# Kernel tuning notes

Hardware: AMD Instinct MI355X
Metric: run time of the kernel (lower is better)

## Reference

```python
import jax, jax.numpy as jnp
import numpy as np

DIM = 1024
HEADS = 16

def setup_inputs() -> dict:
    key = jax.random.key(0)
    ks = jax.random.split(key, 5)
    x = jax.random.normal(ks[0], (4, 2048, DIM), dtype=jnp.float32)
    s = 1.0 / np.sqrt(DIM)
    Wqkv = jax.random.normal(ks[1], (DIM, 3 * DIM), dtype=jnp.float32) * s
    bqkv = jnp.zeros((3 * DIM,), dtype=jnp.float32)
    Wproj = jax.random.normal(ks[2], (DIM, DIM), dtype=jnp.float32) * s
    bproj = jnp.zeros((DIM,), dtype=jnp.float32)
    return {"x": x, "Wqkv": Wqkv, "bqkv": bqkv, "Wproj": Wproj, "bproj": bproj}

def reference(x, Wqkv, bqkv, Wproj, bproj):
    B, N, D = x.shape
    H = HEADS
    hd = D // H
    scale = hd ** (-0.5)
    qkv = x @ Wqkv + bqkv                      # [B, N, 3D]
    q, k, v = jnp.split(qkv, 3, axis=-1)
    # [B, N, H, hd] -> [B, H, N, hd]
    q = q.reshape(B, N, H, hd).transpose(0, 2, 1, 3)
    k = k.reshape(B, N, H, hd).transpose(0, 2, 1, 3)
    v = v.reshape(B, N, H, hd).transpose(0, 2, 1, 3)
    attn = jnp.einsum('bhqd,bhkd->bhqk', q, k) * scale
    attn = jax.nn.softmax(attn, axis=-1)
    out = jnp.einsum('bhqk,bhkd->bhqd', attn, v)
    out = out.transpose(0, 2, 1, 3).reshape(B, N, D)
    return out @ Wproj + bproj
```

## Files before the change

kernel.cpp:

```cpp
#include <hip/hip_runtime.h>
#include <hip/hip_bf16.h>
#include <math.h>


typedef __bf16 bf16;
typedef __bf16 bf16x4 __attribute__((ext_vector_type(4)));
typedef __bf16 bf16x8 __attribute__((ext_vector_type(8)));
typedef float f32x4 __attribute__((ext_vector_type(4)));

#define AS1(p) ((const __attribute__((address_space(1))) void*)(p))
#define AS3(p) ((__attribute__((address_space(3))) void*)(p))

__device__ __forceinline__ void async16(const void* g, void* l) {
    __builtin_amdgcn_global_load_lds(AS1(g), AS3(l), 16, 0, 0);
}

#if __has_builtin(__builtin_amdgcn_exp2f)
#define EXP2(x) __builtin_amdgcn_exp2f(x)
#else
#define EXP2(x) exp2f(x)
#endif

#define QSCALE 0.18033688011112042f


__global__ void cvt_f32_bf16(const float* __restrict__ in, bf16* __restrict__ out, int n4) {
    int i = blockIdx.x * blockDim.x + threadIdx.x;
    if (i < n4) {
        float4 v = ((const float4*)in)[i];
        bf16x4 o;
        o.x = (bf16)v.x; o.y = (bf16)v.y; o.z = (bf16)v.z; o.w = (bf16)v.w;
        ((bf16x4*)out)[i] = o;
    }
}

__global__ void transpose_cvt(const float* __restrict__ in, bf16* __restrict__ out, int K, int N) {
    __shared__ float t[32][33];
    const int n0 = blockIdx.x * 32, k0 = blockIdx.y * 32;
    const int tx = threadIdx.x, ty = threadIdx.y;
    #pragma unroll
    for (int j = 0; j < 32; j += 8)
        t[ty + j][tx] = in[(size_t)(k0 + ty + j) * N + n0 + tx];
    __syncthreads();
    #pragma unroll
    for (int j = 0; j < 32; j += 8)
        out[(size_t)(n0 + ty + j) * K + k0 + tx] = (bf16)t[tx][ty + j];
}


__device__ __forceinline__ void gemm_mainloop(const bf16* __restrict__ A,
                                              const bf16* __restrict__ Bt,
                                              int K, int m0, int n0,
                                              bf16* As, bf16* Bs, f32x4 acc[4][4]) {
    const int tid = threadIdx.x;
    const int wave = tid >> 6, lane = tid & 63;
    const int c = lane & 15, quad = lane >> 4;
    const int wm = (wave & 1) * 64, wn = (wave >> 1) * 64;

    const int ci0 = (wave * 2 + 0) * 64 + lane;
    const int ci1 = (wave * 2 + 1) * 64 + lane;
    const bf16* ga0 = A  + (size_t)(m0 + (ci0 >> 2)) * K + (ci0 & 3) * 8;
    const bf16* ga1 = A  + (size_t)(m0 + (ci1 >> 2)) * K + (ci1 & 3) * 8;
    const bf16* gb0 = Bt + (size_t)(n0 + (ci0 >> 2)) * K + (ci0 & 3) * 8;
    const bf16* gb1 = Bt + (size_t)(n0 + (ci1 >> 2)) * K + (ci1 & 3) * 8;
    bf16* la0 = As + (wave * 2 + 0) * 512;
    bf16* la1 = As + (wave * 2 + 1) * 512;
    bf16* lb0 = Bs + (wave * 2 + 0) * 512;
    bf16* lb1 = Bs + (wave * 2 + 1) * 512;

    for (int kt = 0; kt < K; kt += 32) {
        async16(ga0 + kt, la0);
        async16(ga1 + kt, la1);
        async16(gb0 + kt, lb0);
        async16(gb1 + kt, lb1);
        __syncthreads();
        bf16x8 af[4], bfr[4];
        #pragma unroll
        for (int i = 0; i < 4; i++)
            af[i] = *(const bf16x8*)(As + (wm + i * 16 + c) * 32 + quad * 8);
        #pragma unroll
        for (int j = 0; j < 4; j++)
            bfr[j] = *(const bf16x8*)(Bs + (wn + j * 16 + c) * 32 + quad * 8);
        #pragma unroll
        for (int i = 0; i < 4; i++)
            #pragma unroll
            for (int j = 0; j < 4; j++)
                acc[i][j] = __builtin_amdgcn_mfma_f32_16x16x32_bf16(af[i], bfr[j], acc[i][j], 0, 0, 0);
        __syncthreads();
    }
}


__global__ __launch_bounds__(256) void gemm_qkv(const bf16* __restrict__ A,
                                                const bf16* __restrict__ Bt,
                                                const float* __restrict__ bias,
                                                bf16* __restrict__ Qb,
                                                bf16* __restrict__ Kb,
                                                bf16* __restrict__ Vtb) {
    __shared__ __align__(16) bf16 As[128 * 32];
    __shared__ __align__(16) bf16 Bs[128 * 32];
    f32x4 acc[4][4] = {};
    const int m0 = blockIdx.x * 128, n0 = blockIdx.y * 128;
    gemm_mainloop(A, Bt, 1024, m0, n0, As, Bs, acc);

    const int tid = threadIdx.x;
    const int wave = tid >> 6, lane = tid & 63;
    const int c = lane & 15, quad = lane >> 4;
    const int wm = (wave & 1) * 64, wn = (wave >> 1) * 64;
    const int sel = n0 >> 10;
    bf16* QK = (sel == 0) ? Qb : Kb;
    const float qs = (sel == 0) ? QSCALE : 1.0f;

    #pragma unroll
    for (int j = 0; j < 4; j++) {
        const int nfull = n0 + wn + j * 16 + c;
        const int nmod = nfull & 1023;
        const int h = nmod >> 6, e = nmod & 63;
        const float bv = bias[nfull];
        #pragma unroll
        for (int i = 0; i < 4; i++) {
            const int mbase = m0 + wm + i * 16 + quad * 4;
            const int b = mbase >> 11, t = mbase & 2047;
            if (sel < 2) {
                bf16* dst = QK + (((size_t)(b * 16 + h) * 2048 + t) * 64 + e);
                #pragma unroll
                for (int r = 0; r < 4; r++)
                    dst[(size_t)r * 64] = (bf16)((acc[i][j][r] + bv) * qs);
            } else {
                bf16* dst = Vtb + ((size_t)(b * 16 + h) * 64 + e) * 2048 + t;
                bf16x4 v;
                v.x = (bf16)(acc[i][j][0] + bv);
                v.y = (bf16)(acc[i][j][1] + bv);
                v.z = (bf16)(acc[i][j][2] + bv);
                v.w = (bf16)(acc[i][j][3] + bv);
                *(bf16x4*)dst = v;
            }
        }
    }
}


#define ATTN_STAGE(B) do { \
    async16(kS0, kD0_##B); async16(kS1, kD1_##B); \
    async16(vS0, vD0_##B); async16(vS1, vD1_##B); \
    kS0 += 4096; kS1 += 4096; vS0 += 64; vS1 += 64; \
} while (0)

#define ATTN_COMPUTE(B) do { \
    _Pragma("unroll") \
    for (int j = 0; j < 4; j++) { \
        bf16x8 kf0 = *(const bf16x8*)(kb0_##B + j * 1024); \
        bf16x8 kf1 = *(const bf16x8*)(kb1_##B + j * 1024); \
        f32x4 s0 = {}, s1 = {}; \
        __builtin_amdgcn_s_setprio(1); \
        s0 = __builtin_amdgcn_mfma_f32_16x16x32_bf16(kf0, qf[0][0], s0, 0, 0, 0); \
        s0 = __builtin_amdgcn_mfma_f32_16x16x32_bf16(kf1, qf[0][1], s0, 0, 0, 0); \
        s1 = __builtin_amdgcn_mfma_f32_16x16x32_bf16(kf0, qf[1][0], s1, 0, 0, 0); \
        s1 = __builtin_amdgcn_mfma_f32_16x16x32_bf16(kf1, qf[1][1], s1, 0, 0, 0); \
        __builtin_amdgcn_s_setprio(0); \
        _Pragma("unroll") \
        for (int r = 0; r < 4; r++) { s0[r] = EXP2(s0[r]); s1[r] = EXP2(s1[r]); } \
        lsum[0] += s0; \
        lsum[1] += s1; \
        bf16x4 p0, p1; \
        p0.x = (bf16)s0[0]; p0.y = (bf16)s0[1]; p0.z = (bf16)s0[2]; p0.w = (bf16)s0[3]; \
        p1.x = (bf16)s1[0]; p1.y = (bf16)s1[1]; p1.z = (bf16)s1[2]; p1.w = (bf16)s1[3]; \
        *(bf16x4*)(pwa + j * 16) = p0; \
        *(bf16x4*)(pwb + j * 16) = p1; \
    } \
    _Pragma("unroll") \
    for (int gks = 0; gks < 2; gks++) { \
        const bf16* vbg = gks ? vb1_##B : vb0_##B; \
        bf16x8 vf[4]; \
        _Pragma("unroll") \
        for (int n2 = 0; n2 < 4; n2++) \
            vf[n2] = *(const bf16x8*)(vbg + n2 * 1024); \
        bf16x8 pf0 = *(const bf16x8*)(pra + gks * 32); \
        bf16x8 pf1 = *(const bf16x8*)(prb + gks * 32); \
        __builtin_amdgcn_s_setprio(1); \
        _Pragma("unroll") \
        for (int n2 = 0; n2 < 4; n2++) { \
            o[0][n2] = __builtin_amdgcn_mfma_f32_16x16x32_bf16(pf0, vf[n2], o[0][n2], 0, 0, 0); \
            o[1][n2] = __builtin_amdgcn_mfma_f32_16x16x32_bf16(pf1, vf[n2], o[1][n2], 0, 0, 0); \
        } \
        __builtin_amdgcn_s_setprio(0); \
    } \
} while (0)

__global__ __launch_bounds__(256, 3) void attn_kernel(const bf16* __restrict__ Q,
                                                      const bf16* __restrict__ Kg,
                                                      const bf16* __restrict__ Vt,
                                                      bf16* __restrict__ Out) {
    __shared__ __align__(16) bf16 Ks0[64 * 64];
    __shared__ __align__(16) bf16 Ks1[64 * 64];
    __shared__ __align__(16) bf16 Vs0[64 * 64];
    __shared__ __align__(16) bf16 Vs1[64 * 64];
    __shared__ __align__(16) bf16 Pl[4 * 2 * 16 * 72];

    const int bh = blockIdx.x, qt = blockIdx.y;
    const int tid = threadIdx.x;
    const int wave = tid >> 6, lane = tid & 63;
    const int c = lane & 15, quad = lane >> 4;

    const bf16* Qb = Q + (size_t)bh * 2048 * 64;
    bf16* pw = Pl + wave * 2304;

    const int qbase = qt * 128 + wave * 32;

    bf16x8 qf[2][2];
    #pragma unroll
    for (int i = 0; i < 2; i++)
        #pragma unroll
        for (int ks = 0; ks < 2; ks++)
            qf[i][ks] = *(const bf16x8*)(Qb + (size_t)(qbase + i * 16 + c) * 64 + ks * 32 + quad * 8);

    const int s0i = tid, s1i = 256 + tid;
    const int rk0 = s0i >> 3, cg0 = (s0i & 7) ^ (rk0 & 7);
    const int rk1 = s1i >> 3, cg1 = (s1i & 7) ^ (rk1 & 7);
    const bf16* kS0 = Kg + (size_t)bh * 2048 * 64 + rk0 * 64 + cg0 * 8;
    const bf16* kS1 = Kg + (size_t)bh * 2048 * 64 + rk1 * 64 + cg1 * 8;
    const bf16* vS0 = Vt + (size_t)bh * 64 * 2048 + (size_t)rk0 * 2048 + cg0 * 8;
    const bf16* vS1 = Vt + (size_t)bh * 64 * 2048 + (size_t)rk1 * 2048 + cg1 * 8;
    bf16* kD0_0 = Ks0 + (size_t)(wave * 64) * 8;
    bf16* kD1_0 = Ks0 + (size_t)(256 + wave * 64) * 8;
    bf16* kD0_1 = Ks1 + (size_t)(wave * 64) * 8;
    bf16* kD1_1 = Ks1 + (size_t)(256 + wave * 64) * 8;
    bf16* vD0_0 = Vs0 + (size_t)(wave * 64) * 8;
    bf16* vD1_0 = Vs0 + (size_t)(256 + wave * 64) * 8;
    bf16* vD0_1 = Vs1 + (size_t)(wave * 64) * 8;
    bf16* vD1_1 = Vs1 + (size_t)(256 + wave * 64) * 8;

    const int sw = c & 7;
    const int ch0 = (quad ^ sw) * 8, ch1 = ((quad ^ sw) ^ 4) * 8;
    const bf16* kb0_0 = Ks0 + c * 64 + ch0;
    const bf16* kb1_0 = Ks0 + c * 64 + ch1;
    const bf16* kb0_1 = Ks1 + c * 64 + ch0;
    const bf16* kb1_1 = Ks1 + c * 64 + ch1;
    const bf16* vb0_0 = Vs0 + c * 64 + ch0;
    const bf16* vb1_0 = Vs0 + c * 64 + ch1;
    const bf16* vb0_1 = Vs1 + c * 64 + ch0;
    const bf16* vb1_1 = Vs1 + c * 64 + ch1;
    bf16* pwa = pw + c * 72 + quad * 4;
    bf16* pwb = pwa + 16 * 72;
    const bf16* pra = pw + c * 72 + quad * 8;
    const bf16* prb = pra + 16 * 72;

    f32x4 lsum[2] = {};
    f32x4 o[2][4] = {};

    ATTN_STAGE(0);
    __syncthreads();
    for (int kv2 = 0; kv2 < 16; kv2++) {
        ATTN_STAGE(1);
        ATTN_COMPUTE(0);
        __syncthreads();
        if (kv2 < 15) ATTN_STAGE(0);
        ATTN_COMPUTE(1);
        __syncthreads();
    }

    const int b = bh >> 4, hh = bh & 15;
    #pragma unroll
    for (int i = 0; i < 2; i++) {
        float lh = (lsum[i][0] + lsum[i][1]) + (lsum[i][2] + lsum[i][3]);
        lh += __shfl_xor(lh, 16);
        lh += __shfl_xor(lh, 32);
        const float li0 = __shfl(lh, quad * 4 + 0);
        const float li1 = __shfl(lh, quad * 4 + 1);
        const float li2 = __shfl(lh, quad * 4 + 2);
        const float li3 = __shfl(lh, quad * 4 + 3);
        const float inv[4] = {1.f / li0, 1.f / li1, 1.f / li2, 1.f / li3};
        #pragma unroll
        for (int r = 0; r < 4; r++) {
            const int token = b * 2048 + qbase + i * 16 + quad * 4 + r;
            #pragma unroll
            for (int n2 = 0; n2 < 4; n2++) {
                const int feat = hh * 64 + n2 * 16 + c;
                Out[(size_t)token * 1024 + feat] = (bf16)(o[i][n2][r] * inv[r]);
            }
        }
    }
}


__global__ __launch_bounds__(256) void gemm_proj(const bf16* __restrict__ A,
                                                 const bf16* __restrict__ Bt,
                                                 const float* __restrict__ bias,
                                                 float* __restrict__ Out) {
    __shared__ __align__(16) bf16 As[128 * 32];
    __shared__ __align__(16) bf16 Bs[128 * 32];
    f32x4 acc[4][4] = {};
    const int m0 = blockIdx.x * 128, n0 = blockIdx.y * 128;
    gemm_mainloop(A, Bt, 1024, m0, n0, As, Bs, acc);

    const int tid = threadIdx.x;
    const int wave = tid >> 6, lane = tid & 63;
    const int c = lane & 15, quad = lane >> 4;
    const int wm = (wave & 1) * 64, wn = (wave >> 1) * 64;

    #pragma unroll
    for (int j = 0; j < 4; j++) {
        const int nn = n0 + wn + j * 16 + c;
        const float bv = bias[nn];
        #pragma unroll
        for (int i = 0; i < 4; i++) {
            const int m = m0 + wm + i * 16 + quad * 4;
            #pragma unroll
            for (int r = 0; r < 4; r++)
                Out[(size_t)(m + r) * 1024 + nn] = acc[i][j][r] + bv;
        }
    }
}


extern "C" void kernel_launch(void* const* d_in, const int* in_sizes, int n_in,
                              void* d_out, int out_size, void* d_ws, size_t ws_size,
                              hipStream_t stream) {
    const float* x     = (const float*)d_in[0];
    const float* Wqkv  = (const float*)d_in[1];
    const float* bqkv  = (const float*)d_in[2];
    const float* Wproj = (const float*)d_in[3];
    const float* bproj = (const float*)d_in[4];
    float* out = (float*)d_out;

    char* ws = (char*)d_ws;
    bf16* xb     = (bf16*)(ws);
    bf16* wqkvt  = (bf16*)(ws + 16777216);
    bf16* wprojt = (bf16*)(ws + 23068672);
    bf16* Qb     = (bf16*)(ws + 25165824);
    bf16* Kb     = (bf16*)(ws + 41943040);
    bf16* Vtb    = (bf16*)(ws + 58720256);
    bf16* attno  = xb;

    cvt_f32_bf16<<<8192, 256, 0, stream>>>(x, xb, 2097152);
    transpose_cvt<<<dim3(96, 32), dim3(32, 8), 0, stream>>>(Wqkv, wqkvt, 1024, 3072);
    transpose_cvt<<<dim3(32, 32), dim3(32, 8), 0, stream>>>(Wproj, wprojt, 1024, 1024);
    gemm_qkv<<<dim3(64, 24), 256, 0, stream>>>(xb, wqkvt, bqkv, Qb, Kb, Vtb);
    attn_kernel<<<dim3(64, 16), 256, 0, stream>>>(Qb, Kb, Vtb, attno);
    gemm_proj<<<dim3(64, 8), 256, 0, stream>>>(attno, wprojt, bproj, out);
}
```

Baseline: 272.2 us.

## Double-buffer LDS tiles in GEMM mainloop to overlap loads with MFMA

The shared GEMM mainloop used by the QKV and projection kernels now keeps two LDS buffers for each of A and B. It issues the async global-to-LDS loads for the next K-slab before running the MFMAs on the current one, with the loop unrolled by two. This is meant to hide global load latency behind compute, where before each iteration waited on its own loads. In exchange, each block uses twice as much LDS, which may lower occupancy, and the overlap depends on the compiler placing the vmcnt wait at the barrier.

After: 272.6 us. About the same (+0.1%).

```diff
diff --git a/kernel.cpp b/kernel.cpp
--- a/kernel.cpp
+++ b/kernel.cpp
@@ -48,10 +48,32 @@
 }
 
 
+#define GEMM_STAGE(B) do { \
+    async16(ga0, la0_##B); async16(ga1, la1_##B); \
+    async16(gb0, lb0_##B); async16(gb1, lb1_##B); \
+    ga0 += 32; ga1 += 32; gb0 += 32; gb1 += 32; \
+} while (0)
+
+#define GEMM_COMPUTE(B) do { \
+    bf16x8 af[4], bfr[4]; \
+    _Pragma("unroll") \
+    for (int i = 0; i < 4; i++) \
+        af[i] = *(const bf16x8*)(As##B + (wm + i * 16 + c) * 32 + quad * 8); \
+    _Pragma("unroll") \
+    for (int j = 0; j < 4; j++) \
+        bfr[j] = *(const bf16x8*)(Bs##B + (wn + j * 16 + c) * 32 + quad * 8); \
+    _Pragma("unroll") \
+    for (int i = 0; i < 4; i++) \
+        _Pragma("unroll") \
+        for (int j = 0; j < 4; j++) \
+            acc[i][j] = __builtin_amdgcn_mfma_f32_16x16x32_bf16(af[i], bfr[j], acc[i][j], 0, 0, 0); \
+} while (0)
+
 __device__ __forceinline__ void gemm_mainloop(const bf16* __restrict__ A,
                                               const bf16* __restrict__ Bt,
                                               int K, int m0, int n0,
-                                              bf16* As, bf16* Bs, f32x4 acc[4][4]) {
+                                              bf16* As0, bf16* As1,
+                                              bf16* Bs0, bf16* Bs1, f32x4 acc[4][4]) {
     const int tid = threadIdx.x;
     const int wave = tid >> 6, lane = tid & 63;
     const int c = lane & 15, quad = lane >> 4;
@@ -63,29 +85,24 @@
     const bf16* ga1 = A  + (size_t)(m0 + (ci1 >> 2)) * K + (ci1 & 3) * 8;
     const bf16* gb0 = Bt + (size_t)(n0 + (ci0 >> 2)) * K + (ci0 & 3) * 8;
     const bf16* gb1 = Bt + (size_t)(n0 + (ci1 >> 2)) * K + (ci1 & 3) * 8;
-    bf16* la0 = As + (wave * 2 + 0) * 512;
-    bf16* la1 = As + (wave * 2 + 1) * 512;
-    bf16* lb0 = Bs + (wave * 2 + 0) * 512;
-    bf16* lb1 = Bs + (wave * 2 + 1) * 512;
-
-    for (int kt = 0; kt < K; kt += 32) {
-        async16(ga0 + kt, la0);
-        async16(ga1 + kt, la1);
-        async16(gb0 + kt, lb0);
-        async16(gb1 + kt, lb1);
+    bf16* la0_0 = As0 + (wave * 2 + 0) * 512;
+    bf16* la1_0 = As0 + (wave * 2 + 1) * 512;
+    bf16* la0_1 = As1 + (wave * 2 + 0) * 512;
+    bf16* la1_1 = As1 + (wave * 2 + 1) * 512;
+    bf16* lb0_0 = Bs0 + (wave * 2 + 0) * 512;
+    bf16* lb1_0 = Bs0 + (wave * 2 + 1) * 512;
+    bf16* lb0_1 = Bs1 + (wave * 2 + 0) * 512;
+    bf16* lb1_1 = Bs1 + (wave * 2 + 1) * 512;
+
+    const int nIter = K >> 6;
+    GEMM_STAGE(0);
+    __syncthreads();
+    for (int t = 0; t < nIter; t++) {
+        GEMM_STAGE(1);
+        GEMM_COMPUTE(0);
         __syncthreads();
-        bf16x8 af[4], bfr[4];
-        #pragma unroll
-        for (int i = 0; i < 4; i++)
-            af[i] = *(const bf16x8*)(As + (wm + i * 16 + c) * 32 + quad * 8);
-        #pragma unroll
-        for (int j = 0; j < 4; j++)
-            bfr[j] = *(const bf16x8*)(Bs + (wn + j * 16 + c) * 32 + quad * 8);
-        #pragma unroll
-        for (int i = 0; i < 4; i++)
-            #pragma unroll
-            for (int j = 0; j < 4; j++)
-                acc[i][j] = __builtin_amdgcn_mfma_f32_16x16x32_bf16(af[i], bfr[j], acc[i][j], 0, 0, 0);
+        if (t < nIter - 1) GEMM_STAGE(0);
+        GEMM_COMPUTE(1);
         __syncthreads();
     }
 }
@@ -97,11 +114,13 @@
                                                 bf16* __restrict__ Qb,
                                                 bf16* __restrict__ Kb,
                                                 bf16* __restrict__ Vtb) {
-    __shared__ __align__(16) bf16 As[128 * 32];
-    __shared__ __align__(16) bf16 Bs[128 * 32];
+    __shared__ __align__(16) bf16 As0[128 * 32];
+    __shared__ __align__(16) bf16 As1[128 * 32];
+    __shared__ __align__(16) bf16 Bs0[128 * 32];
+    __shared__ __align__(16) bf16 Bs1[128 * 32];
     f32x4 acc[4][4] = {};
     const int m0 = blockIdx.x * 128, n0 = blockIdx.y * 128;
-    gemm_mainloop(A, Bt, 1024, m0, n0, As, Bs, acc);
+    gemm_mainloop(A, Bt, 1024, m0, n0, As0, As1, Bs0, Bs1, acc);
 
     const int tid = threadIdx.x;
     const int wave = tid >> 6, lane = tid & 63;
@@ -287,11 +306,13 @@
                                                  const bf16* __restrict__ Bt,
                                                  const float* __restrict__ bias,
                                                  float* __restrict__ Out) {
-    __shared__ __align__(16) bf16 As[128 * 32];
-    __shared__ __align__(16) bf16 Bs[128 * 32];
+    __shared__ __align__(16) bf16 As0[128 * 32];
+    __shared__ __align__(16) bf16 As1[128 * 32];
+    __shared__ __align__(16) bf16 Bs0[128 * 32];
+    __shared__ __align__(16) bf16 Bs1[128 * 32];
     f32x4 acc[4][4] = {};
     const int m0 = blockIdx.x * 128, n0 = blockIdx.y * 128;
-    gemm_mainloop(A, Bt, 1024, m0, n0, As, Bs, acc);
+    gemm_mainloop(A, Bt, 1024, m0, n0, As0, As1, Bs0, Bs1, acc);
 
     const int tid = threadIdx.x;
     const int wave = tid >> 6, lane = tid & 63;
```
